# Optimization experiments

Hardware: AMD Instinct MI355X
Metric: run time of the kernel (lower is better)

Reference implementation:

```python
import jax, jax.numpy as jnp
import numpy as np
from jax import lax

BN_EPS = 1e-5

def _bn(h, gamma, beta, mean, var):
    # eval-mode BatchNorm over channel axis 1 of (N, C, T, V)
    inv = gamma / jnp.sqrt(var + BN_EPS)
    return h * inv[None, :, None, None] + (beta - mean * inv)[None, :, None, None]

def setup_inputs() -> dict:
    key = jax.random.key(0)
    ks = jax.random.split(key, 8)
    N, C, O, T, V, K = 32, 64, 64, 1024, 25, 9
    x = jax.random.normal(ks[0], (N, C, T, V), jnp.float32)
    A = jax.random.uniform(ks[1], (3, V, V), jnp.float32)
    attn = jnp.ones((3, V, V), jnp.float32)          # graph_attn init to 1
    wg = jax.random.normal(ks[2], (3, O, C), jnp.float32) * 0.05  # three 1x1 convs
    bg = jnp.zeros((3, O), jnp.float32)
    bn1_gamma = jnp.ones((O,), jnp.float32)
    bn1_beta = jnp.zeros((O,), jnp.float32)
    bn1_mean = jax.random.normal(ks[3], (O,), jnp.float32) * 0.1
    bn1_var = jax.random.uniform(ks[4], (O,), jnp.float32) + 0.5
    wt = jax.random.normal(ks[5], (O, O, K, 1), jnp.float32) * 0.05  # temporal conv (9,1)
    bt = jnp.zeros((O,), jnp.float32)
    bn2_gamma = jnp.ones((O,), jnp.float32)
    bn2_beta = jnp.zeros((O,), jnp.float32)
    bn2_mean = jax.random.normal(ks[6], (O,), jnp.float32) * 0.1
    bn2_var = jax.random.uniform(ks[7], (O,), jnp.float32) + 0.5
    return {"x": x, "A": A, "attn": attn, "wg": wg, "bg": bg,
            "bn1_gamma": bn1_gamma, "bn1_beta": bn1_beta, "bn1_mean": bn1_mean, "bn1_var": bn1_var,
            "wt": wt, "bt": bt,
            "bn2_gamma": bn2_gamma, "bn2_beta": bn2_beta, "bn2_mean": bn2_mean, "bn2_var": bn2_var}

def reference(x, A, attn, wg, bg, bn1_gamma, bn1_beta, bn1_mean, bn1_var,
              wt, bt, bn2_gamma, bn2_beta, bn2_mean, bn2_var):
    # ---- GraphConvolution ----
    Aw = A * attn  # (3, V, V)
    h = None
    for s in range(3):  # num_subset = 3 (small fixed loop)
        agg = jnp.einsum('nctw,wv->nctv', x, Aw[s])          # adjacency matmul
        z = jnp.einsum('nctv,oc->notv', agg, wg[s]) + bg[s][None, :, None, None]
        h = z if h is None else h + z
    h = _bn(h, bn1_gamma, bn1_beta, bn1_mean, bn1_var)
    h = h + x                      # gcn residual (identity: in_channels == out_channels)
    y = jax.nn.relu(h)
    # ---- CoTemporalConvolution (clip-equivalent: padded (9,1) conv over T) ----
    z = lax.conv_general_dilated(y, wt, window_strides=(1, 1),
                                 padding=((4, 4), (0, 0)),
                                 dimension_numbers=('NCHW', 'OIHW', 'NCHW'))
    z = z + bt[None, :, None, None]
    z = _bn(z, bn2_gamma, bn2_beta, bn2_mean, bn2_var)
    # ---- block residual (Delay -> identity in clip-equivalent math) ----
    return jax.nn.relu(z + x)
```

## Files before the change

### kernel.cpp

```cpp
#include <hip/hip_runtime.h>
#include <math.h>
#include <stdint.h>

#define BN_EPS 1e-5f

typedef unsigned short u16;
typedef unsigned int u32;
typedef __attribute__((ext_vector_type(8))) short short8;
typedef __attribute__((ext_vector_type(4))) float f32x4;

#define OFF_YCL 0u
#define OFF_AWP 104857600u
#define OFF_WGP 104863744u
#define OFF_WTP 104888320u
#define OFF_C1A 104962048u
#define OFF_C1B 104962304u
#define OFF_C2A 104962560u
#define OFF_C2B 104962816u

__device__ __forceinline__ u16 f2bf(float f) {
    u32 u = __float_as_uint(f);
    u = (u + 0x7FFFu + ((u >> 16) & 1u)) >> 16;
    return (u16)u;
}
__device__ __forceinline__ float bf2f(u16 h) { return __uint_as_float(((u32)h) << 16); }

#define MFMA16(a, b, c) __builtin_amdgcn_mfma_f32_16x16x32_bf16((a), (b), (c), 0, 0, 0)

__global__ void prep_kernel(const float* __restrict__ A, const float* __restrict__ attn,
                            const float* __restrict__ wg, const float* __restrict__ bg,
                            const float* __restrict__ g1, const float* __restrict__ b1,
                            const float* __restrict__ m1, const float* __restrict__ v1,
                            const float* __restrict__ wt, const float* __restrict__ bt,
                            const float* __restrict__ g2, const float* __restrict__ b2,
                            const float* __restrict__ m2, const float* __restrict__ v2,
                            char* __restrict__ ws) {
    const int tid = threadIdx.x;
    u16* awp = (u16*)(ws + OFF_AWP);
    u16* wgp = (u16*)(ws + OFF_WGP);
    u16* wtp = (u16*)(ws + OFF_WTP);
    float* c1a = (float*)(ws + OFF_C1A);
    float* c1b = (float*)(ws + OFF_C1B);
    float* c2a = (float*)(ws + OFF_C2A);
    float* c2b = (float*)(ws + OFF_C2B);

    for (int i = tid; i < 3072; i += 512) {
        int j = i & 7, lane = (i >> 3) & 63, mf = (i >> 9) & 1, s = i >> 10;
        int v = mf * 16 + (lane & 15), w = (lane >> 4) * 8 + j;
        float val = 0.f;
        if (v < 25 && w < 25) val = A[(s * 25 + w) * 25 + v] * attn[(s * 25 + w) * 25 + v];
        awp[i] = f2bf(val);
    }
    for (int i = tid; i < 12288; i += 512) {
        int j = i & 7, lane = (i >> 3) & 63, ot = (i >> 9) & 3, ks = (i >> 11) & 1, s = i >> 12;
        int c = ks * 32 + (lane >> 4) * 8 + j, o = ot * 16 + (lane & 15);
        wgp[i] = f2bf(wg[(s * 64 + o) * 64 + c]);
    }
    for (int i = tid; i < 36864; i += 512) {
        int j = i & 7, lane = (i >> 3) & 63, ot = (i >> 9) & 3, ks = i >> 11;
        int kk = ks * 32 + (lane >> 4) * 8 + j;
        int tap = kk >> 6, c = kk & 63, o = ot * 16 + (lane & 15);
        wtp[i] = f2bf(wt[(o * 64 + c) * 9 + tap]);
    }
    if (tid < 64) {
        int o = tid;
        float inv1 = g1[o] * rsqrtf(v1[o] + BN_EPS);
        float bgsum = bg[o] + bg[64 + o] + bg[128 + o];
        c1a[o] = inv1;
        c1b[o] = bgsum * inv1 + b1[o] - m1[o] * inv1;
        float inv2 = g2[o] * rsqrtf(v2[o] + BN_EPS);
        c2a[o] = inv2;
        c2b[o] = bt[o] * inv2 + b2[o] - m2[o] * inv2;
    }
}

__global__ __launch_bounds__(512, 2) void gcn_kernel(const float* __restrict__ x,
                                                     char* __restrict__ ws) {
    __shared__ u16 xwl[16 * 64 * 32];
    __shared__ u16 aggL[400 * 64];
    const u16* awp = (const u16*)(ws + OFF_AWP);
    const u16* wgp = (const u16*)(ws + OFF_WGP);
    const float* c1a = (const float*)(ws + OFF_C1A);
    const float* c1b = (const float*)(ws + OFF_C1B);
    u16* ycl = (u16*)(ws + OFF_YCL);

    const int tid = threadIdx.x;
    const int lane = tid & 63;
    const int wv = tid >> 6;
    const int n = blockIdx.y, tb = blockIdx.x;
    const int t0 = tb * 16;

    short8 a1[6];
#pragma unroll
    for (int i = 0; i < 6; ++i) a1[i] = *(const short8*)(awp + (i * 64 + lane) * 8);

    float sa[4], sb[4];
#pragma unroll
    for (int ot = 0; ot < 4; ++ot) {
        int o = ot * 16 + (lane & 15);
        sa[ot] = c1a[o];
        sb[ot] = c1b[o];
    }

    const size_t xbase = (size_t)n * 64 * 1024 * 25;
    for (int e = tid; e < 25600; e += 512) {
        int t = e / 1600, rem = e - t * 1600;
        int c = rem / 25, v = rem - c * 25;
        float xv = x[xbase + ((size_t)c * 1024 + (t0 + t)) * 25 + v];
        xwl[((t * 64 + c) * 32 + v) ^ ((c & 3) << 3)] = f2bf(xv);
    }
    for (int e = tid; e < 16 * 64 * 7; e += 512) {
        int t = e / 448, rem = e - t * 448;
        int c = rem / 7, v = 25 + (rem - c * 7);
        xwl[((t * 64 + c) * 32 + v) ^ ((c & 3) << 3)] = 0;
    }
    __syncthreads();

    f32x4 acc[4][4];
#pragma unroll
    for (int i = 0; i < 4; ++i)
#pragma unroll
        for (int j = 0; j < 4; ++j) acc[i][j] = {0.f, 0.f, 0.f, 0.f};

    const int mfl[4] = {wv, wv + 8, wv + 16, 24};

#pragma unroll
    for (int s = 0; s < 3; ++s) {
#pragma unroll
        for (int i = 0; i < 2; ++i) {
            const int t = wv * 2 + i;
            f32x4 d[2][4];
#pragma unroll
            for (int mf = 0; mf < 2; ++mf)
#pragma unroll
                for (int nf = 0; nf < 4; ++nf) d[mf][nf] = {0.f, 0.f, 0.f, 0.f};
#pragma unroll
            for (int nf = 0; nf < 4; ++nf) {
                int c = nf * 16 + (lane & 15);
                int w0 = (lane >> 4) * 8;
                short8 b = *(const short8*)&xwl[((t * 64 + c) * 32 + w0) ^ ((c & 3) << 3)];
                d[0][nf] = MFMA16(a1[s * 2 + 0], b, d[0][nf]);
                d[1][nf] = MFMA16(a1[s * 2 + 1], b, d[1][nf]);
            }
#pragma unroll
            for (int mf = 0; mf < 2; ++mf)
#pragma unroll
                for (int nf = 0; nf < 4; ++nf)
#pragma unroll
                    for (int r = 0; r < 4; ++r) {
                        int v = mf * 16 + (lane >> 4) * 4 + r;
                        if (v < 25) {
                            int row = t * 25 + v;
                            int c = nf * 16 + (lane & 15);
                            aggL[(row * 64 + c) ^ ((row & 7) << 3)] = f2bf(d[mf][nf][r]);
                        }
                    }
        }
        __syncthreads();
        short8 bw[2][4];
#pragma unroll
        for (int ks = 0; ks < 2; ++ks)
#pragma unroll
            for (int ot = 0; ot < 4; ++ot)
                bw[ks][ot] = *(const short8*)(wgp + (((s * 2 + ks) * 4 + ot) * 64 + lane) * 8);
#pragma unroll
        for (int ks = 0; ks < 2; ++ks)
#pragma unroll
            for (int p = 0; p < 4; ++p) {
                int col = mfl[p] * 16 + (lane & 15);
                int c0 = ks * 32 + (lane >> 4) * 8;
                short8 a = *(const short8*)&aggL[(col * 64 + c0) ^ ((col & 7) << 3)];
#pragma unroll
                for (int ot = 0; ot < 4; ++ot) acc[p][ot] = MFMA16(a, bw[ks][ot], acc[p][ot]);
            }
        __syncthreads();
    }

#pragma unroll
    for (int p = 0; p < 4; ++p) {
        if (p < 3 || wv == 0) {
            int mf = mfl[p];
#pragma unroll
            for (int ot = 0; ot < 4; ++ot) {
                int o = ot * 16 + (lane & 15);
#pragma unroll
                for (int r = 0; r < 4; ++r) {
                    int row = mf * 16 + (lane >> 4) * 4 + r;
                    int tl = row / 25, v = row - tl * 25;
                    float xr = bf2f(xwl[((tl * 64 + o) * 32 + v) ^ ((o & 3) << 3)]);
                    float val = fmaf(acc[p][ot][r], sa[ot], sb[ot]) + xr;
                    val = fmaxf(val, 0.f);
                    aggL[(row * 64 + o) ^ ((row & 7) << 3)] = f2bf(val);
                }
            }
        }
    }
    __syncthreads();
    const size_t ybase = ((size_t)n * 25600 + (size_t)t0 * 25) * 64;
    for (int idx = tid; idx < 3200; idx += 512) {
        int row = idx >> 3, cg = idx & 7;
        short8 vv = *(const short8*)&aggL[(row * 64 + cg * 8) ^ ((row & 7) << 3)];
        *(short8*)(ycl + ybase + row * 64 + cg * 8) = vv;
    }
}

__global__ __launch_bounds__(512, 2) void tcn_kernel(const float* __restrict__ x,
                                                     char* __restrict__ ws,
                                                     float* __restrict__ out) {
    __shared__ u16 ytile[712 * 64];
    const u16* ycl = (const u16*)(ws + OFF_YCL);
    const u16* wtp = (const u16*)(ws + OFF_WTP);
    const float* c2a = (const float*)(ws + OFF_C2A);
    const float* c2b = (const float*)(ws + OFF_C2B);

    const int tid = threadIdx.x, lane = tid & 63, wv = tid >> 6;
    const int n = blockIdx.y, cb = blockIdx.x;
    const int col0 = cb * 512;
    const u16* yn = ycl + (size_t)n * 25600 * 64;

    short8 B0[3][4], B1[3][4];
#pragma unroll
    for (int k3 = 0; k3 < 3; ++k3)
#pragma unroll
        for (int ot = 0; ot < 4; ++ot)
            B0[k3][ot] = *(const short8*)(wtp + ((k3 * 4 + ot) * 64 + lane) * 8);

    float sa[4], sb[4];
#pragma unroll
    for (int ot = 0; ot < 4; ++ot) {
        int o = ot * 16 + (lane & 15);
        sa[ot] = c2a[o];
        sb[ot] = c2b[o];
    }

    for (int idx = tid; idx < 5696; idx += 512) {
        int st = idx >> 3, cg = idx & 7;
        int gcol = col0 - 100 + st;
        short8 v = {0, 0, 0, 0, 0, 0, 0, 0};
        if (gcol >= 0 && gcol < 25600) v = *(const short8*)(yn + (size_t)gcol * 64 + cg * 8);
        *(short8*)&ytile[(st * 64 + cg * 8) ^ ((st & 7) << 3)] = v;
    }
    __syncthreads();

    f32x4 acc[4][4];
#pragma unroll
    for (int i = 0; i < 4; ++i)
#pragma unroll
        for (int j = 0; j < 4; ++j) acc[i][j] = {0.f, 0.f, 0.f, 0.f};

    const int st0 = wv * 64 + (lane & 15);
    const int c0g = (lane >> 4) * 8;

#pragma unroll
    for (int cc = 0; cc < 6; ++cc) {
        if (cc < 5) {
            auto& Bn = (cc & 1) ? B0 : B1;
#pragma unroll
            for (int k3 = 0; k3 < 3; ++k3)
#pragma unroll
                for (int ot = 0; ot < 4; ++ot)
                    Bn[k3][ot] =
                        *(const short8*)(wtp + ((((cc + 1) * 3 + k3) * 4 + ot) * 64 + lane) * 8);
        }
        auto& Bc = (cc & 1) ? B1 : B0;
#pragma unroll
        for (int k3 = 0; k3 < 3; ++k3) {
            const int ks = cc * 3 + k3;
            const int tap = ks >> 1;
            const int c0 = (ks & 1) * 32 + c0g;
            short8 Af[4];
#pragma unroll
            for (int mf = 0; mf < 4; ++mf) {
                int st = st0 + mf * 16 + tap * 25;
                Af[mf] = *(const short8*)&ytile[(st * 64 + c0) ^ ((st & 7) << 3)];
            }
#pragma unroll
            for (int mf = 0; mf < 4; ++mf)
#pragma unroll
                for (int ot = 0; ot < 4; ++ot)
                    acc[mf][ot] = MFMA16(Af[mf], Bc[k3][ot], acc[mf][ot]);
        }
    }

    const size_t obase = (size_t)n * 64 * 25600;
#pragma unroll
    for (int mf = 0; mf < 4; ++mf)
#pragma unroll
        for (int ot = 0; ot < 4; ++ot) {
            int o = ot * 16 + (lane & 15);
            size_t rowb = obase + (size_t)o * 25600 +
                          (size_t)(col0 + wv * 64 + mf * 16 + (lane >> 4) * 4);
            f32x4 xv = *(const f32x4*)(x + rowb);
            f32x4 r;
#pragma unroll
            for (int e = 0; e < 4; ++e)
                r[e] = fmaxf(fmaf(acc[mf][ot][e], sa[ot], sb[ot]) + xv[e], 0.f);
            *(f32x4*)(out + rowb) = r;
        }
}

extern "C" void kernel_launch(void* const* d_in, const int* in_sizes, int n_in,
                              void* d_out, int out_size, void* d_ws, size_t ws_size,
                              hipStream_t stream) {
    const float* x = (const float*)d_in[0];
    const float* A = (const float*)d_in[1];
    const float* attn = (const float*)d_in[2];
    const float* wg = (const float*)d_in[3];
    const float* bg = (const float*)d_in[4];
    const float* g1 = (const float*)d_in[5];
    const float* b1 = (const float*)d_in[6];
    const float* m1 = (const float*)d_in[7];
    const float* v1 = (const float*)d_in[8];
    const float* wt = (const float*)d_in[9];
    const float* bt = (const float*)d_in[10];
    const float* g2 = (const float*)d_in[11];
    const float* b2 = (const float*)d_in[12];
    const float* m2 = (const float*)d_in[13];
    const float* v2 = (const float*)d_in[14];
    char* ws = (char*)d_ws;
    float* out = (float*)d_out;

    hipLaunchKernelGGL(prep_kernel, dim3(1), dim3(512), 0, stream, A, attn, wg, bg, g1, b1, m1,
                       v1, wt, bt, g2, b2, m2, v2, ws);
    hipLaunchKernelGGL(gcn_kernel, dim3(64, 32), dim3(512), 0, stream, x, ws);
    hipLaunchKernelGGL(tcn_kernel, dim3(50, 32), dim3(512), 0, stream, x, ws, out);
}
```

Measured before the change: 760.2 us.

## Halve GCN and TCN tiles to raise occupancy, vectorize x loads

Both kernels now process half the rows per block (8 time steps in GCN, 256 columns in TCN), shrinking LDS and register footprints so launch bounds can request 4 blocks per CU. The GCN x tile load now uses contiguous float4 reads instead of scalar strided gathers. The TCN weight prefetch becomes a single rolling 4-fragment double buffer in a non-unrolled loop. The trade-off is more halo re-reads in TCN (100-column halo over 256 instead of 512 columns) and less per-wave MFMA work to hide latency.

New measurement: 762.3 us. No clear change (+0.3%).

```diff
diff --git a/kernel.cpp b/kernel.cpp
--- a/kernel.cpp
+++ b/kernel.cpp
@@ -74,10 +74,10 @@
     }
 }
 
-__global__ __launch_bounds__(512, 2) void gcn_kernel(const float* __restrict__ x,
+__global__ __launch_bounds__(512, 4) void gcn_kernel(const float* __restrict__ x,
                                                      char* __restrict__ ws) {
-    __shared__ u16 xwl[16 * 64 * 32];
-    __shared__ u16 aggL[400 * 64];
+    __shared__ u16 xwl[8 * 64 * 32];
+    __shared__ u16 aggL[208 * 64];
     const u16* awp = (const u16*)(ws + OFF_AWP);
     const u16* wgp = (const u16*)(ws + OFF_WGP);
     const float* c1a = (const float*)(ws + OFF_C1A);
@@ -88,7 +88,7 @@
     const int lane = tid & 63;
     const int wv = tid >> 6;
     const int n = blockIdx.y, tb = blockIdx.x;
-    const int t0 = tb * 16;
+    const int t0 = tb * 8;
 
     short8 a1[6];
 #pragma unroll
@@ -102,61 +102,46 @@
         sb[ot] = c1b[o];
     }
 
-    const size_t xbase = (size_t)n * 64 * 1024 * 25;
-    for (int e = tid; e < 25600; e += 512) {
-        int t = e / 1600, rem = e - t * 1600;
-        int c = rem / 25, v = rem - c * 25;
-        float xv = x[xbase + ((size_t)c * 1024 + (t0 + t)) * 25 + v];
-        xwl[((t * 64 + c) * 32 + v) ^ ((c & 3) << 3)] = f2bf(xv);
-    }
-    for (int e = tid; e < 16 * 64 * 7; e += 512) {
-        int t = e / 448, rem = e - t * 448;
+    const size_t xbase = (size_t)n * 64 * 25600;
+    for (int idx = tid; idx < 3200; idx += 512) {
+        int c = idx / 50, r4 = idx - c * 50;
+        f32x4 xv = *(const f32x4*)(x + xbase + (size_t)c * 25600 + t0 * 25 + r4 * 4);
+#pragma unroll
+        for (int e = 0; e < 4; ++e) {
+            int tr = r4 * 4 + e;
+            int t = tr / 25, v = tr - t * 25;
+            xwl[((t * 64 + c) * 32 + v) ^ ((c & 3) << 3)] = f2bf(xv[e]);
+        }
+    }
+    for (int idx = tid; idx < 3584; idx += 512) {
+        int t = idx / 448, rem = idx - t * 448;
         int c = rem / 7, v = 25 + (rem - c * 7);
         xwl[((t * 64 + c) * 32 + v) ^ ((c & 3) << 3)] = 0;
     }
     __syncthreads();
 
-    f32x4 acc[4][4];
-#pragma unroll
-    for (int i = 0; i < 4; ++i)
+    f32x4 acc[2][4];
+#pragma unroll
+    for (int i = 0; i < 2; ++i)
 #pragma unroll
         for (int j = 0; j < 4; ++j) acc[i][j] = {0.f, 0.f, 0.f, 0.f};
 
-    const int mfl[4] = {wv, wv + 8, wv + 16, 24};
-
 #pragma unroll
     for (int s = 0; s < 3; ++s) {
-#pragma unroll
-        for (int i = 0; i < 2; ++i) {
-            const int t = wv * 2 + i;
-            f32x4 d[2][4];
-#pragma unroll
-            for (int mf = 0; mf < 2; ++mf)
-#pragma unroll
-                for (int nf = 0; nf < 4; ++nf) d[mf][nf] = {0.f, 0.f, 0.f, 0.f};
-#pragma unroll
-            for (int nf = 0; nf < 4; ++nf) {
-                int c = nf * 16 + (lane & 15);
-                int w0 = (lane >> 4) * 8;
-                short8 b = *(const short8*)&xwl[((t * 64 + c) * 32 + w0) ^ ((c & 3) << 3)];
-                d[0][nf] = MFMA16(a1[s * 2 + 0], b, d[0][nf]);
-                d[1][nf] = MFMA16(a1[s * 2 + 1], b, d[1][nf]);
-            }
-#pragma unroll
-            for (int mf = 0; mf < 2; ++mf)
-#pragma unroll
-                for (int nf = 0; nf < 4; ++nf)
-#pragma unroll
-                    for (int r = 0; r < 4; ++r) {
-                        int v = mf * 16 + (lane >> 4) * 4 + r;
-                        if (v < 25) {
-                            int row = t * 25 + v;
-                            int c = nf * 16 + (lane & 15);
-                            aggL[(row * 64 + c) ^ ((row & 7) << 3)] = f2bf(d[mf][nf][r]);
-                        }
-                    }
-        }
-        __syncthreads();
+        const int t = wv;
+        f32x4 d[2][4];
+#pragma unroll
+        for (int mf = 0; mf < 2; ++mf)
+#pragma unroll
+            for (int nf = 0; nf < 4; ++nf) d[mf][nf] = {0.f, 0.f, 0.f, 0.f};
+#pragma unroll
+        for (int nf = 0; nf < 4; ++nf) {
+            int c = nf * 16 + (lane & 15);
+            int w0 = (lane >> 4) * 8;
+            short8 b = *(const short8*)&xwl[((t * 64 + c) * 32 + w0) ^ ((c & 3) << 3)];
+            d[0][nf] = MFMA16(a1[s * 2 + 0], b, d[0][nf]);
+            d[1][nf] = MFMA16(a1[s * 2 + 1], b, d[1][nf]);
+        }
         short8 bw[2][4];
 #pragma unroll
         for (int ks = 0; ks < 2; ++ks)
@@ -164,50 +149,67 @@
             for (int ot = 0; ot < 4; ++ot)
                 bw[ks][ot] = *(const short8*)(wgp + (((s * 2 + ks) * 4 + ot) * 64 + lane) * 8);
 #pragma unroll
-        for (int ks = 0; ks < 2; ++ks)
-#pragma unroll
-            for (int p = 0; p < 4; ++p) {
-                int col = mfl[p] * 16 + (lane & 15);
+        for (int mf = 0; mf < 2; ++mf)
+#pragma unroll
+            for (int nf = 0; nf < 4; ++nf)
+#pragma unroll
+                for (int r = 0; r < 4; ++r) {
+                    int v = mf * 16 + (lane >> 4) * 4 + r;
+                    if (v < 25) {
+                        int row = t * 25 + v;
+                        int c = nf * 16 + (lane & 15);
+                        aggL[(row * 64 + c) ^ ((row & 7) << 3)] = f2bf(d[mf][nf][r]);
+                    }
+                }
+        __syncthreads();
+#pragma unroll
+        for (int p = 0; p < 2; ++p) {
+            if (p == 1 && wv >= 5) break;
+            int mfr = (p == 0) ? wv : (8 + wv);
+            int col = mfr * 16 + (lane & 15);
+#pragma unroll
+            for (int ks = 0; ks < 2; ++ks) {
                 int c0 = ks * 32 + (lane >> 4) * 8;
                 short8 a = *(const short8*)&aggL[(col * 64 + c0) ^ ((col & 7) << 3)];
 #pragma unroll
                 for (int ot = 0; ot < 4; ++ot) acc[p][ot] = MFMA16(a, bw[ks][ot], acc[p][ot]);
             }
+        }
         __syncthreads();
     }
 
 #pragma unroll
-    for (int p = 0; p < 4; ++p) {
-        if (p < 3 || wv == 0) {
-            int mf = mfl[p];
-#pragma unroll
-            for (int ot = 0; ot < 4; ++ot) {
-                int o = ot * 16 + (lane & 15);
-#pragma unroll
-                for (int r = 0; r < 4; ++r) {
-                    int row = mf * 16 + (lane >> 4) * 4 + r;
+    for (int p = 0; p < 2; ++p) {
+        if (p == 1 && wv >= 5) break;
+        int mfr = (p == 0) ? wv : (8 + wv);
+#pragma unroll
+        for (int ot = 0; ot < 4; ++ot) {
+            int o = ot * 16 + (lane & 15);
+#pragma unroll
+            for (int r = 0; r < 4; ++r) {
+                int row = mfr * 16 + (lane >> 4) * 4 + r;
+                if (row < 200) {
                     int tl = row / 25, v = row - tl * 25;
                     float xr = bf2f(xwl[((tl * 64 + o) * 32 + v) ^ ((o & 3) << 3)]);
                     float val = fmaf(acc[p][ot][r], sa[ot], sb[ot]) + xr;
-                    val = fmaxf(val, 0.f);
-                    aggL[(row * 64 + o) ^ ((row & 7) << 3)] = f2bf(val);
+                    aggL[(row * 64 + o) ^ ((row & 7) << 3)] = f2bf(fmaxf(val, 0.f));
                 }
             }
         }
     }
     __syncthreads();
     const size_t ybase = ((size_t)n * 25600 + (size_t)t0 * 25) * 64;
-    for (int idx = tid; idx < 3200; idx += 512) {
+    for (int idx = tid; idx < 1600; idx += 512) {
         int row = idx >> 3, cg = idx & 7;
         short8 vv = *(const short8*)&aggL[(row * 64 + cg * 8) ^ ((row & 7) << 3)];
         *(short8*)(ycl + ybase + row * 64 + cg * 8) = vv;
     }
 }
 
-__global__ __launch_bounds__(512, 2) void tcn_kernel(const float* __restrict__ x,
+__global__ __launch_bounds__(512, 4) void tcn_kernel(const float* __restrict__ x,
                                                      char* __restrict__ ws,
                                                      float* __restrict__ out) {
-    __shared__ u16 ytile[712 * 64];
+    __shared__ u16 ytile[456 * 64];
     const u16* ycl = (const u16*)(ws + OFF_YCL);
     const u16* wtp = (const u16*)(ws + OFF_WTP);
     const float* c2a = (const float*)(ws + OFF_C2A);
@@ -215,15 +217,8 @@
 
     const int tid = threadIdx.x, lane = tid & 63, wv = tid >> 6;
     const int n = blockIdx.y, cb = blockIdx.x;
-    const int col0 = cb * 512;
+    const int col0 = cb * 256;
     const u16* yn = ycl + (size_t)n * 25600 * 64;
-
-    short8 B0[3][4], B1[3][4];
-#pragma unroll
-    for (int k3 = 0; k3 < 3; ++k3)
-#pragma unroll
-        for (int ot = 0; ot < 4; ++ot)
-            B0[k3][ot] = *(const short8*)(wtp + ((k3 * 4 + ot) * 64 + lane) * 8);
 
     float sa[4], sb[4];
 #pragma unroll
@@ -233,63 +228,59 @@
         sb[ot] = c2b[o];
     }
 
-    for (int idx = tid; idx < 5696; idx += 512) {
+    for (int idx = tid; idx < 3648; idx += 512) {
         int st = idx >> 3, cg = idx & 7;
         int gcol = col0 - 100 + st;
         short8 v = {0, 0, 0, 0, 0, 0, 0, 0};
         if (gcol >= 0 && gcol < 25600) v = *(const short8*)(yn + (size_t)gcol * 64 + cg * 8);
         *(short8*)&ytile[(st * 64 + cg * 8) ^ ((st & 7) << 3)] = v;
     }
+
+    short8 Bc[4], Bn[4];
+#pragma unroll
+    for (int ot = 0; ot < 4; ++ot) Bc[ot] = *(const short8*)(wtp + (ot * 64 + lane) * 8);
+
     __syncthreads();
 
-    f32x4 acc[4][4];
-#pragma unroll
-    for (int i = 0; i < 4; ++i)
+    f32x4 acc[2][4];
+#pragma unroll
+    for (int i = 0; i < 2; ++i)
 #pragma unroll
         for (int j = 0; j < 4; ++j) acc[i][j] = {0.f, 0.f, 0.f, 0.f};
 
-    const int st0 = wv * 64 + (lane & 15);
+    const int st0 = wv * 32 + (lane & 15);
     const int c0g = (lane >> 4) * 8;
 
-#pragma unroll
-    for (int cc = 0; cc < 6; ++cc) {
-        if (cc < 5) {
-            auto& Bn = (cc & 1) ? B0 : B1;
-#pragma unroll
-            for (int k3 = 0; k3 < 3; ++k3)
-#pragma unroll
-                for (int ot = 0; ot < 4; ++ot)
-                    Bn[k3][ot] =
-                        *(const short8*)(wtp + ((((cc + 1) * 3 + k3) * 4 + ot) * 64 + lane) * 8);
-        }
-        auto& Bc = (cc & 1) ? B1 : B0;
-#pragma unroll
-        for (int k3 = 0; k3 < 3; ++k3) {
-            const int ks = cc * 3 + k3;
-            const int tap = ks >> 1;
-            const int c0 = (ks & 1) * 32 + c0g;
-            short8 Af[4];
-#pragma unroll
-            for (int mf = 0; mf < 4; ++mf) {
-                int st = st0 + mf * 16 + tap * 25;
-                Af[mf] = *(const short8*)&ytile[(st * 64 + c0) ^ ((st & 7) << 3)];
-            }
-#pragma unroll
-            for (int mf = 0; mf < 4; ++mf)
-#pragma unroll
-                for (int ot = 0; ot < 4; ++ot)
-                    acc[mf][ot] = MFMA16(Af[mf], Bc[k3][ot], acc[mf][ot]);
-        }
+    for (int ks = 0; ks < 18; ++ks) {
+        if (ks < 17) {
+#pragma unroll
+            for (int ot = 0; ot < 4; ++ot)
+                Bn[ot] = *(const short8*)(wtp + (((ks + 1) * 4 + ot) * 64 + lane) * 8);
+        }
+        const int tap = ks >> 1;
+        const int c0 = (ks & 1) * 32 + c0g;
+        short8 Af[2];
+#pragma unroll
+        for (int mf = 0; mf < 2; ++mf) {
+            int st = st0 + mf * 16 + tap * 25;
+            Af[mf] = *(const short8*)&ytile[(st * 64 + c0) ^ ((st & 7) << 3)];
+        }
+#pragma unroll
+        for (int mf = 0; mf < 2; ++mf)
+#pragma unroll
+            for (int ot = 0; ot < 4; ++ot) acc[mf][ot] = MFMA16(Af[mf], Bc[ot], acc[mf][ot]);
+#pragma unroll
+        for (int ot = 0; ot < 4; ++ot) Bc[ot] = Bn[ot];
     }
 
     const size_t obase = (size_t)n * 64 * 25600;
 #pragma unroll
-    for (int mf = 0; mf < 4; ++mf)
+    for (int mf = 0; mf < 2; ++mf)
 #pragma unroll
         for (int ot = 0; ot < 4; ++ot) {
             int o = ot * 16 + (lane & 15);
             size_t rowb = obase + (size_t)o * 25600 +
-                          (size_t)(col0 + wv * 64 + mf * 16 + (lane >> 4) * 4);
+                          (size_t)(col0 + wv * 32 + mf * 16 + (lane >> 4) * 4);
             f32x4 xv = *(const f32x4*)(x + rowb);
             f32x4 r;
 #pragma unroll
@@ -322,6 +313,6 @@
 
     hipLaunchKernelGGL(prep_kernel, dim3(1), dim3(512), 0, stream, A, attn, wg, bg, g1, b1, m1,
                        v1, wt, bt, g2, b2, m2, v2, ws);
-    hipLaunchKernelGGL(gcn_kernel, dim3(64, 32), dim3(512), 0, stream, x, ws);
-    hipLaunchKernelGGL(tcn_kernel, dim3(50, 32), dim3(512), 0, stream, x, ws, out);
-}
+    hipLaunchKernelGGL(gcn_kernel, dim3(128, 32), dim3(512), 0, stream, x, ws);
+    hipLaunchKernelGGL(tcn_kernel, dim3(100, 32), dim3(512), 0, stream, x, ws, out);
+}
```
